# Performance work log

Hardware: AMD Instinct MI355X
Metric: run time of the kernel (lower is better)

The kernel has to match this reference:

```python
import jax, jax.numpy as jnp
import numpy as np

B, L, D = 8, 2048, 1024
NH = 16            # n_head
HD = D // NH       # 64; attention is (HD x HD) per token in this module


def setup_inputs() -> dict:
    key = jax.random.key(0)
    ks = jax.random.split(key, 5)
    s = 0.02  # init scale for weights
    return {
        "x": jax.random.normal(ks[0], (B, L, D), jnp.float32),
        "Wq": jax.random.normal(ks[1], (D, D), jnp.float32) * s,
        "bq": jnp.zeros((D,), jnp.float32),
        "Wk": jax.random.normal(ks[2], (D, D), jnp.float32) * s,
        "bk": jnp.zeros((D,), jnp.float32),
        "Wv": jax.random.normal(ks[3], (D, D), jnp.float32) * s,
        "bv": jnp.zeros((D,), jnp.float32),
        "Wo": jax.random.normal(ks[4], (D, D), jnp.float32) * s,
        "bo": jnp.zeros((D,), jnp.float32),
    }


def reference(x, Wq, bq, Wk, bk, Wv, bv, Wo, bo):
    b, l, d = x.shape
    # QKV projections
    q = (x @ Wq + bq).reshape(b, l, HD, NH)
    k = (x @ Wk + bk).reshape(b, l, HD, NH)
    v = (x @ Wv + bv).reshape(b, l, HD, NH)
    # NOTE: module reshapes to (b, l, head_dim, n_head), so scores are
    # per-token (HD, HD) with the NH axis contracted; norm = sqrt(NH).
    norm = jnp.sqrt(jnp.asarray(NH, x.dtype))
    attn = jnp.einsum('blij,blkj->blik', q, k) / norm  # (b, l, HD, HD)
    attn = attn + 1e-06
    # mask = tril of the VALUES; jnp.where uses nonzero-as-True semantics.
    mask = jnp.tril(attn)
    attn = jnp.where(mask, attn, -jnp.inf)
    probs = jax.nn.softmax(attn, axis=-1)
    y = jnp.einsum('blik,blkj->blij', probs, v).reshape(b, l, d)
    return y @ Wo + bo
```

## Files before the change

kernel.cpp:

```cpp
#include <hip/hip_runtime.h>
#include <hip/hip_bf16.h>
#include <stdint.h>

typedef unsigned short u16;

#define Bdim 8
#define Ldim 2048
#define Ddim 1024
#define NH 16
#define HD 64
#define MTOK (Bdim*Ldim)

typedef __bf16 bf16x8 __attribute__((ext_vector_type(8)));
typedef float  f32x4  __attribute__((ext_vector_type(4)));
typedef float  f32x16 __attribute__((ext_vector_type(16)));

#define AS1 __attribute__((address_space(1)))
#define AS3 __attribute__((address_space(3)))

__device__ __forceinline__ void gload_lds16(const void* g, void* l) {
  __builtin_amdgcn_global_load_lds((const AS1 void*)g, (AS3 void*)l, 16, 0, 0);
}

__device__ __forceinline__ u16 f2bf(float f) {
  uint32_t u = __builtin_bit_cast(uint32_t, f);
  u += 0x7fffu + ((u >> 16) & 1u);
  return (u16)(u >> 16);
}
__device__ __forceinline__ uint32_t pkpair(float lo, float hi) {
  return (uint32_t)f2bf(lo) | ((uint32_t)f2bf(hi) << 16);
}

__global__ __launch_bounds__(256) void conv_f32_bf16(const float* __restrict__ in,
                                                     u16* __restrict__ out, int n4) {
  int i = blockIdx.x * 256 + threadIdx.x;
  if (i < n4) {
    float4 v = ((const float4*)in)[i];
    uint32_t w0 = (uint32_t)f2bf(v.x) | ((uint32_t)f2bf(v.y) << 16);
    uint32_t w1 = (uint32_t)f2bf(v.z) | ((uint32_t)f2bf(v.w) << 16);
    ((uint2*)out)[i] = make_uint2(w0, w1);
  }
}

__global__ __launch_bounds__(256) void conv_transpose_w(const float* __restrict__ W,
                                                        u16* __restrict__ Wt) {
  __shared__ float t[32][33];
  int tx = threadIdx.x & 31, ty = threadIdx.x >> 5;
  int k0 = blockIdx.x * 32, n0 = blockIdx.y * 32;
  #pragma unroll
  for (int i = 0; i < 32; i += 8)
    t[ty + i][tx] = W[(size_t)(k0 + ty + i) * Ddim + n0 + tx];
  __syncthreads();
  #pragma unroll
  for (int i = 0; i < 32; i += 8)
    Wt[(size_t)(n0 + ty + i) * Ddim + k0 + tx] = f2bf(t[tx][ty + i]);
}

template <int FUSED>
__global__ __launch_bounds__(512, 2) void gemm8p(const u16* __restrict__ A,
                                                 const u16* __restrict__ Bt,
                                                 const float* __restrict__ b0p,
                                                 const float* __restrict__ b1p,
                                                 const float* __restrict__ b2p,
                                                 void* __restrict__ o0,
                                                 void* __restrict__ o1,
                                                 void* __restrict__ o2) {
  __shared__ alignas(16) u16 LP[65536];
  const int tid = threadIdx.x;
  const int wid = tid >> 6, lane = tid & 63;
  const int wr = wid >> 2, wc = wid & 3;
  const int fr = lane & 15, fh = lane >> 4;

  const int bid = blockIdx.x;
  const int xcd = bid & 7, idx = bid >> 3;
  const int mt = xcd * 8 + (idx & 7);
  const int nt = idx >> 3;
  const int m0 = mt * 256, n0g = nt * 256;

  const int x7 = fr & 7;
  const int cks0 = (fh ^ x7) * 8;
  const int cks1 = ((4 + fh) ^ x7) * 8;
  const int rA = (wr * 128 + fr) * 64;
  const int rB = (wc * 64 + fr) * 64;

  const int srt = tid >> 3;
  const int sgc = ((tid & 7) ^ (srt & 7)) * 8;
  const u16* aSt = A  + (size_t)(m0  + srt) * 1024 + sgc;
  const u16* bSt = Bt + (size_t)(n0g + srt) * 1024 + sgc;

#define RDA4(DST, B_, KS_, MH_) do {                                           \
    const u16* p_ = LP + (B_) * 16384 + rA + (MH_) * 4096 + ((KS_) ? cks1 : cks0); \
    DST[0] = *(const bf16x8*)(p_);                                             \
    DST[1] = *(const bf16x8*)(p_ + 1024);                                      \
    DST[2] = *(const bf16x8*)(p_ + 2048);                                      \
    DST[3] = *(const bf16x8*)(p_ + 3072);                                      \
  } while (0)
#define RDB4(DST, B_, KS_) do {                                                \
    const u16* p_ = LP + 32768 + (B_) * 16384 + rB + ((KS_) ? cks1 : cks0);    \
    DST[0] = *(const bf16x8*)(p_);                                             \
    DST[1] = *(const bf16x8*)(p_ + 1024);                                      \
    DST[2] = *(const bf16x8*)(p_ + 2048);                                      \
    DST[3] = *(const bf16x8*)(p_ + 3072);                                      \
  } while (0)
#define STGH(ISB_, T_, H_, B_) do {                                            \
    const u16* s_ = ((ISB_) ? bSt : aSt) + (size_t)(H_) * 131072 + (size_t)(T_) * 64; \
    u16* d_ = (u16*)LP + ((ISB_) ? 32768 : 0) + (B_) * 16384 + (H_) * 8192 + (wid << 9); \
    gload_lds16(s_, d_);                                                       \
    gload_lds16(s_ + 65536, d_ + 4096);                                        \
  } while (0)
#define MFMA16(AF, BF, MH) do {                                                \
    __builtin_amdgcn_s_setprio(1);                                             \
    _Pragma("unroll")                                                          \
    for (int mm_ = 0; mm_ < 4; ++mm_)                                          \
      _Pragma("unroll")                                                        \
      for (int n_ = 0; n_ < 4; ++n_)                                           \
        acc[(MH) * 4 + mm_][n_] = __builtin_amdgcn_mfma_f32_16x16x32_bf16(     \
            AF[mm_], BF[n_], acc[(MH) * 4 + mm_][n_], 0, 0, 0);                \
    __builtin_amdgcn_s_setprio(0);                                             \
  } while (0)
#define WAITV(N) asm volatile("s_waitcnt vmcnt(" #N ")" ::: "memory")
#define BAR() do { asm volatile("" ::: "memory");                              \
                   __builtin_amdgcn_s_barrier();                               \
                   asm volatile("" ::: "memory"); } while (0)

  f32x4 acc[8][4] = {};
  bf16x8 aA[4], aB[4], bA[4], bB[4];

  STGH(1, 0, 0, 0); STGH(0, 0, 0, 0); STGH(1, 0, 1, 0); STGH(0, 0, 1, 0);
  STGH(1, 1, 0, 1); STGH(0, 1, 0, 1);
  WAITV(4);
  BAR();
  RDA4(aA, 0, 0, 0); RDB4(bA, 0, 0);

  #pragma unroll 1
  for (int i = 0; i < 8; ++i) {
    const int u1 = 2 * i + 1;
    const int s2 = (i < 7) ? 2 * i + 2 : 14;
    const int s3 = (i < 7) ? 2 * i + 3 : 15;
    RDA4(aB, 0, 0, 1);                 STGH(1, u1, 1, 1);
    BAR(); MFMA16(aA, bA, 0); BAR();
    RDA4(aA, 0, 1, 0); RDB4(bB, 0, 1); STGH(0, u1, 1, 1);
    BAR(); MFMA16(aB, bA, 1); BAR();
    RDA4(aB, 0, 1, 1);                 STGH(1, s2, 0, 0);
    BAR(); MFMA16(aA, bB, 0); WAITV(2); BAR();
    RDA4(aA, 1, 0, 0); RDB4(bA, 1, 0); STGH(0, s2, 0, 0);
    BAR(); MFMA16(aB, bB, 1); BAR();
    RDA4(aB, 1, 0, 1);                 STGH(1, s2, 1, 0);
    BAR(); MFMA16(aA, bA, 0); BAR();
    RDA4(aA, 1, 1, 0); RDB4(bB, 1, 1); STGH(0, s2, 1, 0);
    BAR(); MFMA16(aB, bA, 1); BAR();
    RDA4(aB, 1, 1, 1);                 STGH(1, s3, 0, 1);
    BAR(); MFMA16(aA, bB, 0); WAITV(2); BAR();
    RDA4(aA, 0, 0, 0); RDB4(bA, 0, 0); STGH(0, s3, 0, 1);
    BAR(); MFMA16(aB, bB, 1); BAR();
  }
  __syncthreads();

  if (FUSED) {
    const int which = nt >> 2;
    const int n0l = (nt & 3) * 256;
    const float* bias = which == 0 ? b0p : which == 1 ? b1p : b2p;
    u16* Out = (u16*)(which == 0 ? o0 : which == 1 ? o1 : o2);
    u16* Ct = LP;
    #pragma unroll 1
    for (int h = 0; h < 2; ++h) {
      if (h) __syncthreads();
      if (wr == h) {
        #pragma unroll
        for (int n = 0; n < 4; ++n) {
          float bvv = bias[n0l + wc * 64 + n * 16 + fr];
          #pragma unroll
          for (int m = 0; m < 8; ++m)
            #pragma unroll
            for (int r = 0; r < 4; ++r)
              Ct[wc * 9216 + (m * 16 + fh * 4 + r) * 72 + n * 16 + fr] =
                  f2bf(acc[m][n][r] + bvv);
        }
      }
      __syncthreads();
      if (which != 2) {
        #pragma unroll
        for (int j = 0; j < 8; ++j) {
          int r = j * 16 + (tid >> 5), c8 = tid & 31;
          uint4 v = *(const uint4*)(Ct + (c8 >> 3) * 9216 + r * 72 + (c8 & 7) * 8);
          *(uint4*)(Out + (size_t)(m0 + h * 128 + r) * Ddim + n0l + c8 * 8) = v;
        }
      } else {
        #pragma unroll
        for (int j = 0; j < 4; ++j) {
          int q = j * 512 + tid, r = q >> 4, ii = q & 15;
          u16 tmp[16];
          #pragma unroll
          for (int jj = 0; jj < 16; ++jj) {
            int c = ii + 16 * jj;
            tmp[jj] = Ct[(c >> 6) * 9216 + r * 72 + (c & 63)];
          }
          u16* dst = Out + (size_t)(m0 + h * 128 + r) * Ddim + ii * 64 + (n0l >> 4);
          *(uint4*)dst = *(uint4*)tmp;
          *(uint4*)(dst + 8) = *(uint4*)(tmp + 8);
        }
      }
      __syncthreads();
    }
  } else {
    float* Cf = (float*)LP;
    float* Out = (float*)o0;
    #pragma unroll 1
    for (int h = 0; h < 4; ++h) {
      if (h) __syncthreads();
      if (wr == (h >> 1) && (wc >> 1) == (h & 1)) {
        #pragma unroll
        for (int n = 0; n < 4; ++n) {
          float bvv = b0p[n0g + (h & 1) * 128 + (wc & 1) * 64 + n * 16 + fr];
          #pragma unroll
          for (int m = 0; m < 8; ++m)
            #pragma unroll
            for (int r = 0; r < 4; ++r)
              Cf[(wc & 1) * 8704 + (m * 16 + fh * 4 + r) * 68 + n * 16 + fr] =
                  acc[m][n][r] + bvv;
        }
      }
      __syncthreads();
      #pragma unroll
      for (int j = 0; j < 8; ++j) {
        int r = j * 16 + (tid >> 5), c4 = tid & 31;
        float4 v = *(const float4*)(Cf + (c4 >> 4) * 8704 + r * 68 + (c4 & 15) * 4);
        *(float4*)(Out + (size_t)(m0 + (h >> 1) * 128 + r) * Ddim +
                   n0g + (h & 1) * 128 + c4 * 4) = v;
      }
      __syncthreads();
    }
  }
#undef RDA4
#undef RDB4
#undef STGH
#undef MFMA16
#undef WAITV
#undef BAR
}

__global__ __launch_bounds__(256) void attn_mfma(const u16* __restrict__ Q,
                                                 const u16* __restrict__ Kb,
                                                 const u16* __restrict__ Vt,
                                                 u16* __restrict__ Y) {
  const int wid = threadIdx.x >> 6, lane = threadIdx.x & 63;
  const int tok = blockIdx.x * 4 + wid;
  const size_t base = (size_t)tok * Ddim;
  const int hi = lane >> 5, c31 = lane & 31;

  const bf16x8 kf0 = *(const bf16x8*)(Kb + base + (size_t)c31 * NH + hi * 8);
  const bf16x8 kf1 = *(const bf16x8*)(Kb + base + (size_t)(32 + c31) * NH + hi * 8);
  const bf16x8 qf0 = *(const bf16x8*)(Q  + base + (size_t)c31 * NH + hi * 8);
  const bf16x8 qf1 = *(const bf16x8*)(Q  + base + (size_t)(32 + c31) * NH + hi * 8);
  bf16x8 bv[4];
  #pragma unroll
  for (int c = 0; c < 4; ++c)
    bv[c] = *(const bf16x8*)(Vt + base + (size_t)(lane & 15) * HD + c * 16 + hi * 8);

  const f32x16 z = {};
  f32x16 s00 = __builtin_amdgcn_mfma_f32_32x32x16_bf16(kf0, qf0, z, 0, 0, 0);
  f32x16 s01 = __builtin_amdgcn_mfma_f32_32x32x16_bf16(kf0, qf1, z, 0, 0, 0);
  f32x16 s11 = __builtin_amdgcn_mfma_f32_32x32x16_bf16(kf1, qf1, z, 0, 0, 0);

  float a[16], b0[16], b1[16];
  float mA = -3e38f, mB = -3e38f;
  #pragma unroll
  for (int r = 0; r < 16; ++r) {
    const int kl = (r & 3) + 8 * (r >> 2) + 4 * hi;
    const bool keep = kl <= c31;
    float v00 = fmaf(s00[r], 0.25f, 1e-6f);
    float v01 = fmaf(s01[r], 0.25f, 1e-6f);
    float v11 = fmaf(s11[r], 0.25f, 1e-6f);
    a[r]  = keep ? v00 : -3e38f;
    b0[r] = v01;
    b1[r] = keep ? v11 : -3e38f;
    mA = fmaxf(mA, a[r]);
    mB = fmaxf(mB, fmaxf(b0[r], b1[r]));
  }
  mA = fmaxf(mA, __shfl_xor(mA, 32, 64));
  mB = fmaxf(mB, __shfl_xor(mB, 32, 64));
  float sA = 0.f, sB = 0.f;
  #pragma unroll
  for (int r = 0; r < 16; ++r) {
    a[r]  = __expf(a[r]  - mA);  sA += a[r];
    b0[r] = __expf(b0[r] - mB);
    b1[r] = __expf(b1[r] - mB);  sB += b0[r] + b1[r];
  }
  sA += __shfl_xor(sA, 32, 64);
  sB += __shfl_xor(sB, 32, 64);
  const float iA = __builtin_amdgcn_rcpf(sA);
  const float iB = __builtin_amdgcn_rcpf(sB);

  uint32_t pA[4][2], pB0[4][2], pB1[4][2];
  #pragma unroll
  for (int m = 0; m < 4; ++m)
    #pragma unroll
    for (int t = 0; t < 2; ++t) {
      pA [m][t] = pkpair(a [4*m+2*t] * iA, a [4*m+2*t+1] * iA);
      pB0[m][t] = pkpair(b0[4*m+2*t] * iB, b0[4*m+2*t+1] * iB);
      pB1[m][t] = pkpair(b1[4*m+2*t] * iB, b1[4*m+2*t+1] * iB);
    }

#define AFRAG(dst, src, cp) do {                                              \
    uint32_t k0_ = hi ? src[2*(cp)+1][0] : src[2*(cp)][0];                    \
    uint32_t k1_ = hi ? src[2*(cp)+1][1] : src[2*(cp)][1];                    \
    uint32_t s0_ = hi ? src[2*(cp)][0]   : src[2*(cp)+1][0];                  \
    uint32_t s1_ = hi ? src[2*(cp)][1]   : src[2*(cp)+1][1];                  \
    uint32_t r0_ = (uint32_t)__shfl_xor((int)s0_, 32, 64);                    \
    uint32_t r1_ = (uint32_t)__shfl_xor((int)s1_, 32, 64);                    \
    union { uint32_t w[4]; bf16x8 v; } u_;                                    \
    u_.w[0] = hi ? r0_ : k0_;  u_.w[1] = hi ? r1_ : k1_;                      \
    u_.w[2] = hi ? k0_ : r0_;  u_.w[3] = hi ? k1_ : r1_;                      \
    dst = u_.v;                                                               \
  } while (0)

  f32x16 y0 = {}, y1 = {};
  bf16x8 af;
  AFRAG(af, pA, 0);  y0 = __builtin_amdgcn_mfma_f32_32x32x16_bf16(af, bv[0], y0, 0, 0, 0);
  AFRAG(af, pA, 1);  y0 = __builtin_amdgcn_mfma_f32_32x32x16_bf16(af, bv[1], y0, 0, 0, 0);
  AFRAG(af, pB0, 0); y1 = __builtin_amdgcn_mfma_f32_32x32x16_bf16(af, bv[0], y1, 0, 0, 0);
  AFRAG(af, pB0, 1); y1 = __builtin_amdgcn_mfma_f32_32x32x16_bf16(af, bv[1], y1, 0, 0, 0);
  AFRAG(af, pB1, 0); y1 = __builtin_amdgcn_mfma_f32_32x32x16_bf16(af, bv[2], y1, 0, 0, 0);
  AFRAG(af, pB1, 1); y1 = __builtin_amdgcn_mfma_f32_32x32x16_bf16(af, bv[3], y1, 0, 0, 0);
#undef AFRAG

  if (c31 < 16) {
    #pragma unroll
    for (int r = 0; r < 16; ++r) {
      const int row = (r & 3) + 8 * (r >> 2) + 4 * hi;
      Y[base + (size_t)row * NH + c31]        = f2bf(y0[r]);
      Y[base + (size_t)(32 + row) * NH + c31] = f2bf(y1[r]);
    }
  }
}

extern "C" void kernel_launch(void* const* d_in, const int* in_sizes, int n_in,
                              void* d_out, int out_size, void* d_ws, size_t ws_size,
                              hipStream_t stream) {
  const float* x  = (const float*)d_in[0];
  const float* Wq = (const float*)d_in[1];
  const float* bq = (const float*)d_in[2];
  const float* Wk = (const float*)d_in[3];
  const float* bk = (const float*)d_in[4];
  const float* Wv = (const float*)d_in[5];
  const float* bv = (const float*)d_in[6];
  const float* Wo = (const float*)d_in[7];
  const float* bo = (const float*)d_in[8];
  float* out = (float*)d_out;

  u16* xb = (u16*)d_ws;
  u16* Wt = xb + (size_t)MTOK * Ddim;
  u16* Qb = Wt + 4ull * Ddim * Ddim;
  u16* Kb = Qb + (size_t)MTOK * Ddim;
  u16* Vb = Kb + (size_t)MTOK * Ddim;
  u16* Yb = xb;

  conv_f32_bf16<<<(MTOK * Ddim / 4 + 255) / 256, 256, 0, stream>>>(x, xb, MTOK * Ddim / 4);

  dim3 tg(Ddim / 32, Ddim / 32);
  conv_transpose_w<<<tg, 256, 0, stream>>>(Wq, Wt + 0ull * Ddim * Ddim);
  conv_transpose_w<<<tg, 256, 0, stream>>>(Wk, Wt + 1ull * Ddim * Ddim);
  conv_transpose_w<<<tg, 256, 0, stream>>>(Wv, Wt + 2ull * Ddim * Ddim);
  conv_transpose_w<<<tg, 256, 0, stream>>>(Wo, Wt + 3ull * Ddim * Ddim);

  gemm8p<1><<<dim3(768), 512, 0, stream>>>(xb, Wt, bq, bk, bv, Qb, Kb, Vb);

  attn_mfma<<<MTOK / 4, 256, 0, stream>>>(Qb, Kb, Vb, Yb);

  gemm8p<0><<<dim3(256), 512, 0, stream>>>(Yb, Wt + 3ull * Ddim * Ddim,
                                           bo, bo, bo, out, out, out);
}
```

Baseline: 209.1 us.

## Restage GEMM LDS tiles by K-half with 4-way swizzle and finer waits

Changes the LDS staging layout of the bf16 GEMM from 64-wide K rows (split by M half) to two 32-wide K-half planes, with an XOR swizzle over four 16-byte chunks. The global-to-LDS loads and fragment reads are remapped to match, and the prefetch schedule now waits on vmcnt more often, once per K-half. The aim is to get finer-grained overlap of global loads with MFMA work and fewer LDS bank conflicts. In exchange, each global row read is shorter, and the extra waits could stall the pipeline.

```diff
diff --git a/kernel.cpp b/kernel.cpp
--- a/kernel.cpp
+++ b/kernel.cpp
@@ -77,36 +77,35 @@
   const int nt = idx >> 3;
   const int m0 = mt * 256, n0g = nt * 256;
 
-  const int x7 = fr & 7;
-  const int cks0 = (fh ^ x7) * 8;
-  const int cks1 = ((4 + fh) ^ x7) * 8;
-  const int rA = (wr * 128 + fr) * 64;
-  const int rB = (wc * 64 + fr) * 64;
-
-  const int srt = tid >> 3;
-  const int sgc = ((tid & 7) ^ (srt & 7)) * 8;
-  const u16* aSt = A  + (size_t)(m0  + srt) * 1024 + sgc;
-  const u16* bSt = Bt + (size_t)(n0g + srt) * 1024 + sgc;
+  const int cks = (fh ^ (fr & 3)) * 8;
+  const int rA = (wr * 128 + fr) * 32;
+  const int rB = (wc * 64 + fr) * 32;
+
+  const int srow = tid >> 2;
+  const int sblk = (tid & 3) ^ (srow & 3);
+  const u16* aSt = A  + (size_t)(m0  + srow) * 1024 + sblk * 8;
+  const u16* bSt = Bt + (size_t)(n0g + srow) * 1024 + sblk * 8;
 
 #define RDA4(DST, B_, KS_, MH_) do {                                           \
-    const u16* p_ = LP + (B_) * 16384 + rA + (MH_) * 4096 + ((KS_) ? cks1 : cks0); \
+    const u16* p_ = LP + (B_) * 16384 + (KS_) * 8192 + rA + (MH_) * 2048 + cks; \
     DST[0] = *(const bf16x8*)(p_);                                             \
-    DST[1] = *(const bf16x8*)(p_ + 1024);                                      \
-    DST[2] = *(const bf16x8*)(p_ + 2048);                                      \
-    DST[3] = *(const bf16x8*)(p_ + 3072);                                      \
+    DST[1] = *(const bf16x8*)(p_ + 512);                                       \
+    DST[2] = *(const bf16x8*)(p_ + 1024);                                      \
+    DST[3] = *(const bf16x8*)(p_ + 1536);                                      \
   } while (0)
 #define RDB4(DST, B_, KS_) do {                                                \
-    const u16* p_ = LP + 32768 + (B_) * 16384 + rB + ((KS_) ? cks1 : cks0);    \
+    const u16* p_ = LP + 32768 + (B_) * 16384 + (KS_) * 8192 + rB + cks;       \
     DST[0] = *(const bf16x8*)(p_);                                             \
-    DST[1] = *(const bf16x8*)(p_ + 1024);                                      \
-    DST[2] = *(const bf16x8*)(p_ + 2048);                                      \
-    DST[3] = *(const bf16x8*)(p_ + 3072);                                      \
-  } while (0)
-#define STGH(ISB_, T_, H_, B_) do {                                            \
-    const u16* s_ = ((ISB_) ? bSt : aSt) + (size_t)(H_) * 131072 + (size_t)(T_) * 64; \
-    u16* d_ = (u16*)LP + ((ISB_) ? 32768 : 0) + (B_) * 16384 + (H_) * 8192 + (wid << 9); \
+    DST[1] = *(const bf16x8*)(p_ + 512);                                       \
+    DST[2] = *(const bf16x8*)(p_ + 1024);                                      \
+    DST[3] = *(const bf16x8*)(p_ + 1536);                                      \
+  } while (0)
+#define STGU(ISB_, KH_, T_, B_) do {                                           \
+    const u16* s_ = ((ISB_) ? bSt : aSt) + (T_) * 64 + (KH_) * 32;             \
+    u16* d_ = (u16*)LP + ((ISB_) ? 32768 : 0) + (B_) * 16384 + (KH_) * 8192 +  \
+              (wid << 9);                                                      \
     gload_lds16(s_, d_);                                                       \
-    gload_lds16(s_ + 65536, d_ + 4096);                                        \
+    gload_lds16(s_ + 131072, d_ + 4096);                                       \
   } while (0)
 #define MFMA16(AF, BF, MH) do {                                                \
     __builtin_amdgcn_s_setprio(1);                                             \
@@ -126,34 +125,36 @@
   f32x4 acc[8][4] = {};
   bf16x8 aA[4], aB[4], bA[4], bB[4];
 
-  STGH(1, 0, 0, 0); STGH(0, 0, 0, 0); STGH(1, 0, 1, 0); STGH(0, 0, 1, 0);
-  STGH(1, 1, 0, 1); STGH(0, 1, 0, 1);
-  WAITV(4);
+  STGU(0, 0, 0, 0); STGU(1, 0, 0, 0);
+  STGU(0, 1, 0, 0); STGU(1, 1, 0, 0);
+  STGU(0, 0, 1, 1); STGU(1, 0, 1, 1);
+  WAITV(8);
   BAR();
   RDA4(aA, 0, 0, 0); RDB4(bA, 0, 0);
 
   #pragma unroll 1
   for (int i = 0; i < 8; ++i) {
     const int u1 = 2 * i + 1;
-    const int s2 = (i < 7) ? 2 * i + 2 : 14;
+    const int s2 = (i < 7) ? 2 * i + 2 : 15;
     const int s3 = (i < 7) ? 2 * i + 3 : 15;
-    RDA4(aB, 0, 0, 1);                 STGH(1, u1, 1, 1);
-    BAR(); MFMA16(aA, bA, 0); BAR();
-    RDA4(aA, 0, 1, 0); RDB4(bB, 0, 1); STGH(0, u1, 1, 1);
+    RDA4(aB, 0, 0, 1);                 STGU(0, 1, u1, 1);
+    BAR(); MFMA16(aA, bA, 0); WAITV(6); BAR();
+    RDA4(aA, 0, 1, 0); RDB4(bB, 0, 1); STGU(1, 1, u1, 1);
     BAR(); MFMA16(aB, bA, 1); BAR();
-    RDA4(aB, 0, 1, 1);                 STGH(1, s2, 0, 0);
-    BAR(); MFMA16(aA, bB, 0); WAITV(2); BAR();
-    RDA4(aA, 1, 0, 0); RDB4(bA, 1, 0); STGH(0, s2, 0, 0);
+    RDA4(aB, 0, 1, 1);                 STGU(0, 0, s2, 0);
+    BAR(); MFMA16(aA, bB, 0); WAITV(6); BAR();
+    RDA4(aA, 1, 0, 0); RDB4(bA, 1, 0); STGU(1, 0, s2, 0);
     BAR(); MFMA16(aB, bB, 1); BAR();
-    RDA4(aB, 1, 0, 1);                 STGH(1, s2, 1, 0);
-    BAR(); MFMA16(aA, bA, 0); BAR();
-    RDA4(aA, 1, 1, 0); RDB4(bB, 1, 1); STGH(0, s2, 1, 0);
+    RDA4(aB, 1, 0, 1);                 STGU(0, 1, s2, 0);
+    BAR(); MFMA16(aA, bA, 0); WAITV(6); BAR();
+    RDA4(aA, 1, 1, 0); RDB4(bB, 1, 1); STGU(1, 1, s2, 0);
     BAR(); MFMA16(aB, bA, 1); BAR();
-    RDA4(aB, 1, 1, 1);                 STGH(1, s3, 0, 1);
-    BAR(); MFMA16(aA, bB, 0); WAITV(2); BAR();
-    RDA4(aA, 0, 0, 0); RDB4(bA, 0, 0); STGH(0, s3, 0, 1);
+    RDA4(aB, 1, 1, 1);                 STGU(0, 0, s3, 1);
+    BAR(); MFMA16(aA, bB, 0); WAITV(6); BAR();
+    RDA4(aA, 0, 0, 0); RDB4(bA, 0, 0); STGU(1, 0, s3, 1);
     BAR(); MFMA16(aB, bB, 1); BAR();
   }
+  WAITV(0);
   __syncthreads();
 
   if (FUSED) {
@@ -233,7 +234,7 @@
   }
 #undef RDA4
 #undef RDB4
-#undef STGH
+#undef STGU
 #undef MFMA16
 #undef WAITV
 #undef BAR
```

Measured after the change: 222.5 us. 1.06x slower.
